# Optimization experiments

Measured on AMD Instinct MI355X. Metric: run time of the kernel, lower is better.

The kernel has to match this reference:

```python
import jax, jax.numpy as jnp
import numpy as np

B, T, D = 256, 512, 32   # batch, seq_len, var_length (== input_size == output_size)
H, L = 256, 2            # hidden_size, num_layers


def setup_inputs() -> dict:
    key = jax.random.key(0)
    ks = jax.random.split(key, 16)
    s = 1.0 / np.sqrt(H)  # PyTorch LSTM/Linear default init range
    def u(k, shape):
        return jax.random.uniform(k, shape, jnp.float32, -s, s)
    inp = {"input": jax.random.normal(ks[0], (B, T, D), jnp.float32)}
    # encoder LSTM (b = b_ih + b_hh folded together); gate order i,f,g,o
    inp["enc_Wih0"] = u(ks[1], (4 * H, D)); inp["enc_Whh0"] = u(ks[2], (4 * H, H)); inp["enc_b0"] = u(ks[3], (4 * H,))
    inp["enc_Wih1"] = u(ks[4], (4 * H, H)); inp["enc_Whh1"] = u(ks[5], (4 * H, H)); inp["enc_b1"] = u(ks[6], (4 * H,))
    # decoder LSTM
    inp["dec_Wih0"] = u(ks[7], (4 * H, D)); inp["dec_Whh0"] = u(ks[8], (4 * H, H)); inp["dec_b0"] = u(ks[9], (4 * H,))
    inp["dec_Wih1"] = u(ks[10], (4 * H, H)); inp["dec_Whh1"] = u(ks[11], (4 * H, H)); inp["dec_b1"] = u(ks[12], (4 * H,))
    # output projection
    inp["fc_W"] = u(ks[13], (D, H)); inp["fc_b"] = u(ks[14], (D,))
    return inp


def _lstm_cell(x, h, c, Wih, Whh, b):
    g = x @ Wih.T + h @ Whh.T + b            # [B, 4H]
    i, f, gg, o = jnp.split(g, 4, axis=-1)   # PyTorch gate order i,f,g,o
    c = jax.nn.sigmoid(f) * c + jax.nn.sigmoid(i) * jnp.tanh(gg)
    h = jax.nn.sigmoid(o) * jnp.tanh(c)
    return h, c


def reference(input, enc_Wih0, enc_Whh0, enc_b0, enc_Wih1, enc_Whh1, enc_b1,
              dec_Wih0, dec_Whh0, dec_b0, dec_Wih1, dec_Whh1, dec_b1, fc_W, fc_b):
    b, t, d = input.shape
    hdim = enc_Whh0.shape[1]
    x = jnp.transpose(input, (1, 0, 2))  # time-major [T, B, D]

    # ----- encoder: 2-layer LSTM, keep final (h, c) per layer -----
    enc = [(enc_Wih0, enc_Whh0, enc_b0), (enc_Wih1, enc_Whh1, enc_b1)]
    hs, cs = [], []
    seq = x
    for Wih, Whh, bb in enc:
        def step(carry, xt, Wih=Wih, Whh=Whh, bb=bb):
            h, c = carry
            h, c = _lstm_cell(xt, h, c, Wih, Whh, bb)
            return (h, c), h
        z = jnp.zeros((b, hdim), input.dtype)
        (hT, cT), seq = jax.lax.scan(step, (z, z), seq)
        hs.append(hT); cs.append(cT)
    h0 = jnp.stack(hs)  # [L, B, H]
    c0 = jnp.stack(cs)

    dec = [(dec_Wih0, dec_Whh0, dec_b0), (dec_Wih1, dec_Whh1, dec_b1)]

    def dec_step(carry, _):
        xt, h, c = carry
        inp_l = xt
        new_h, new_c = [], []
        for l, (Wih, Whh, bb) in enumerate(dec):
            hl, cl = _lstm_cell(inp_l, h[l], c[l], Wih, Whh, bb)
            new_h.append(hl); new_c.append(cl)
            inp_l = hl
        pred = inp_l @ fc_W.T + fc_b  # [B, D]
        return (pred, jnp.stack(new_h), jnp.stack(new_c)), pred

    x0 = jnp.zeros((b, d), input.dtype)
    _, preds = jax.lax.scan(dec_step, (x0, h0, c0), None, length=t)  # [T, B, D]
    # cat along time then reverse (inv_idx)
    out = jnp.transpose(preds, (1, 0, 2))[:, ::-1, :]
    return out
```

## Files before the change

### kernel.cpp

```cpp
#include <hip/hip_runtime.h>

typedef __attribute__((ext_vector_type(8))) short bf16x8;
typedef __attribute__((ext_vector_type(4))) float f32x4;

#define MFMA16(a,b,c) __builtin_amdgcn_mfma_f32_16x16x32_bf16((a),(b),(c),0,0,0)


#define SZ_HBUF   (2*256*256*2)
#define OFF_H0H   0
#define OFF_H0L   (OFF_H0H + SZ_HBUF)
#define OFF_H1H   (OFF_H0L + SZ_HBUF)
#define OFF_H1L   (OFF_H1H + SZ_HBUF)
#define OFF_CFIN  (OFF_H1L + SZ_HBUF)
#define OFF_EW0H  (OFF_CFIN + 524288)
#define OFF_EW0L  (OFF_EW0H + 589824)
#define OFF_EW1H  (OFF_EW0L + 589824)
#define OFF_EW1L  (OFF_EW1H + 1048576)
#define OFF_DW0H  (OFF_EW1L + 1048576)
#define OFF_DW0L  (OFF_DW0H + 1048576)
#define OFF_DW1H  (OFF_DW0L + 1048576)
#define OFF_DW1L  (OFF_DW1H + 1048576)
#define OFF_BEFF  (OFF_DW1L + 1048576)
#define OFF_FCWH  (OFF_BEFF + 4096)
#define OFF_FCWL  (OFF_FCWH + 16384)
#define OFF_EFLG  (OFF_FCWL + 16384)
#define OFF_DFLG  (OFF_EFLG + 4096)

static __device__ __forceinline__ unsigned short f2bf(float f) {
  unsigned u = __float_as_uint(f);
  u = u + 0x7fffu + ((u >> 16) & 1u);
  return (unsigned short)(u >> 16);
}
static __device__ __forceinline__ float bf2f(unsigned short s) {
  return __uint_as_float(((unsigned)s) << 16);
}
static __device__ __forceinline__ float sigf(float x) {
  return 1.f / (1.f + __expf(-x));
}
static __device__ __forceinline__ float tanhsafe(float x) {
  float a = fabsf(x);
  float e = __expf(-2.f * a);
  float t = (1.f - e) / (1.f + e);
  return x < 0.f ? -t : t;
}
static __device__ __forceinline__ void st_hpair(float h, unsigned short* ph, unsigned short* pl) {
  unsigned short hi = f2bf(h);
  unsigned short lo = f2bf(h - bf2f(hi));
  __hip_atomic_store(ph, hi, __ATOMIC_RELAXED, __HIP_MEMORY_SCOPE_AGENT);
  __hip_atomic_store(pl, lo, __ATOMIC_RELAXED, __HIP_MEMORY_SCOPE_AGENT);
}
static __device__ __forceinline__ f32x4 ld16(const void* p) {
  f32x4 d;
  asm volatile("global_load_dwordx4 %0, %1, off sc0 sc1" : "=&v"(d) : "v"(p) : "memory");
  return d;
}
static __device__ __forceinline__ void wait_vm0() {
  asm volatile("s_waitcnt vmcnt(0)" ::: "memory");
  __builtin_amdgcn_sched_barrier(0);
}
static __device__ __forceinline__ void flag_barrier(unsigned* flags, int gc, unsigned round) {
  __syncthreads();
  if (threadIdx.x == 0)
    __hip_atomic_store(flags + gc, round, __ATOMIC_RELAXED, __HIP_MEMORY_SCOPE_AGENT);
  if (threadIdx.x < 64) {
    int l = threadIdx.x;
    for (;;) {
      unsigned v = (l < 16) ? __hip_atomic_load(flags + l, __ATOMIC_RELAXED, __HIP_MEMORY_SCOPE_AGENT)
                            : round;
      if (__all((int)(v >= round))) break;
    }
  }
  __syncthreads();
}

#define LDSF(base, row, kk) \
  (*(const bf16x8*)((base) + ((((row) << 9) | (lrow << 4) | ((kk) << 6)) ^ (((row) & 7) << 4))))

__global__ void k_prep_cat(int nrows, const float* __restrict__ s0, int K0,
                           const float* __restrict__ s1, int K1,
                           unsigned short* __restrict__ whi, unsigned short* __restrict__ wlo) {
  int K = K0 + K1;
  int tot = nrows * K;
  for (int idx = blockIdx.x * blockDim.x + threadIdx.x; idx < tot; idx += gridDim.x * blockDim.x) {
    int n = idx / K, k = idx - n * K;
    float v = (k < K0) ? s0[n * K0 + k] : s1[n * K1 + (k - K0)];
    unsigned short hi = f2bf(v);
    unsigned short lo = f2bf(v - bf2f(hi));
    whi[idx] = hi; wlo[idx] = lo;
  }
}
__global__ void k_prep_dec0(const float* __restrict__ Wih0, const float* __restrict__ Whh0,
                            const float* __restrict__ fcW,
                            unsigned short* __restrict__ whi, unsigned short* __restrict__ wlo) {
  int tot = 1024 * 512;
  for (int idx = blockIdx.x * blockDim.x + threadIdx.x; idx < tot; idx += gridDim.x * blockDim.x) {
    int n = idx >> 9, k = idx & 511;
    float v;
    if (k < 256) {
      v = 0.f;
      #pragma unroll
      for (int d = 0; d < 32; ++d) v += Wih0[n * 32 + d] * fcW[d * 256 + k];
    } else {
      v = Whh0[n * 256 + (k - 256)];
    }
    unsigned short hi = f2bf(v);
    unsigned short lo = f2bf(v - bf2f(hi));
    whi[idx] = hi; wlo[idx] = lo;
  }
}
__global__ void k_prep_beff(const float* __restrict__ Wih0, const float* __restrict__ b0,
                            const float* __restrict__ fcb, float* __restrict__ beff) {
  int n = blockIdx.x * blockDim.x + threadIdx.x;
  if (n < 1024) {
    float v = b0[n];
    #pragma unroll
    for (int d = 0; d < 32; ++d) v += Wih0[n * 32 + d] * fcb[d];
    beff[n] = v;
  }
}

__global__ __launch_bounds__(256, 1)
void k_encoder(const float* __restrict__ input,
               const unsigned short* __restrict__ w0hi, const unsigned short* __restrict__ w0lo,
               const unsigned short* __restrict__ w1hi, const unsigned short* __restrict__ w1lo,
               const float* __restrict__ b0, const float* __restrict__ b1,
               unsigned short* h0h, unsigned short* h0l,
               unsigned short* h1h, unsigned short* h1l,
               float* __restrict__ cfin, unsigned* flags)
{
  const int wg = blockIdx.x;
  const int gb = wg & 15, gc = wg >> 4;
  const int tid = threadIdx.x;
  const int wid = tid >> 6, lane = tid & 63;
  const int lcol = lane & 15, lrow = lane >> 4;
  const int r0 = gb * 16, u0 = gc * 16;
  const int wrow = wid * 256 + u0 + lcol;

  __shared__ char s_h0[2][8192];
  __shared__ char s_h1[2][8192];
  __shared__ float gA[4][16][17];
  __shared__ float gB[4][16][17];
  __shared__ float cb[2][16][16];

  cb[0][tid >> 4][tid & 15] = 0.f;
  cb[1][tid >> 4][tid & 15] = 0.f;

  const int srow = (tid >> 5) & 7;
  const int scol8 = (tid & 31) << 3;
  const int dA = ((srow << 9) | ((tid & 31) << 4)) ^ (srow << 4);
  const int dB = dA + 4096;

  bf16x8 w0h_[9], w0l_[9], w1h_[16], w1l_[16];
  {
    const unsigned short* p = w0hi + (size_t)wrow * 288 + lrow * 8;
    const unsigned short* q = w0lo + (size_t)wrow * 288 + lrow * 8;
    #pragma unroll
    for (int kk = 0; kk < 9; ++kk) {
      w0h_[kk] = *(const bf16x8*)(p + kk * 32);
      w0l_[kk] = *(const bf16x8*)(q + kk * 32);
    }
    const unsigned short* p1 = w1hi + (size_t)wrow * 512 + lrow * 8;
    const unsigned short* q1 = w1lo + (size_t)wrow * 512 + lrow * 8;
    #pragma unroll
    for (int kk = 0; kk < 16; ++kk) {
      w1h_[kk] = *(const bf16x8*)(p1 + kk * 32);
      w1l_[kk] = *(const bf16x8*)(q1 + kk * 32);
    }
  }
  const float bias0 = b0[wrow];
  const float bias1 = b1[wrow];
  unsigned* gflags = flags + gb * 64;
  __syncthreads();

  for (int k = 0; k <= 512; ++k) {
    const int rp = (k - 1) & 1;
    const int wp = k & 1;

    f32x4 ahh = {0.f,0.f,0.f,0.f}, ahl = {0.f,0.f,0.f,0.f}, alh = {0.f,0.f,0.f,0.f};
    union { bf16x8 v; unsigned short s[8]; } xh, xl;
    if (k < 512) {
      const float* px = input + (size_t)(r0 + lcol) * 16384 + (size_t)k * 32 + lrow * 8;
      f32x4 a = *(const f32x4*)px;
      f32x4 b = *(const f32x4*)(px + 4);
      #pragma unroll
      for (int j = 0; j < 4; ++j) {
        unsigned short t1 = f2bf(a[j]); xh.s[j] = t1;     xl.s[j]     = f2bf(a[j] - bf2f(t1));
        unsigned short t2 = f2bf(b[j]); xh.s[4 + j] = t2; xl.s[4 + j] = f2bf(b[j] - bf2f(t2));
      }
    }

    const unsigned short* p0h = h0h + (size_t)rp * 65536 + (size_t)(r0 + srow) * 256 + scol8;
    const unsigned short* p0l = h0l + (size_t)rp * 65536 + (size_t)(r0 + srow) * 256 + scol8;
    const unsigned short* p1h = h1h + (size_t)wp * 65536 + (size_t)(r0 + srow) * 256 + scol8;
    const unsigned short* p1l = h1l + (size_t)wp * 65536 + (size_t)(r0 + srow) * 256 + scol8;
    f32x4 v0 = ld16(p0h), v1 = ld16(p0h + 2048);
    f32x4 v2 = ld16(p0l), v3 = ld16(p0l + 2048);
    f32x4 v4 = ld16(p1h), v5 = ld16(p1h + 2048);
    f32x4 v6 = ld16(p1l), v7 = ld16(p1l + 2048);

    if (k < 512) {
      ahh = MFMA16(xh.v, w0h_[0], ahh);
      ahl = MFMA16(xh.v, w0l_[0], ahl);
      alh = MFMA16(xl.v, w0h_[0], alh);
    }

    wait_vm0();
    *(f32x4*)(s_h0[0] + dA) = v0; *(f32x4*)(s_h0[0] + dB) = v1;
    *(f32x4*)(s_h0[1] + dA) = v2; *(f32x4*)(s_h0[1] + dB) = v3;
    *(f32x4*)(s_h1[0] + dA) = v4; *(f32x4*)(s_h1[0] + dB) = v5;
    *(f32x4*)(s_h1[1] + dA) = v6; *(f32x4*)(s_h1[1] + dB) = v7;
    __syncthreads();

    bf16x8 f0h[8], f0l[8];
    #pragma unroll
    for (int kk = 0; kk < 8; ++kk) {
      f0h[kk] = LDSF(s_h0[0], lcol, kk);
      f0l[kk] = LDSF(s_h0[1], lcol, kk);
    }

    if (k < 512) {
      #pragma unroll
      for (int kk = 0; kk < 8; ++kk) {
        ahh = MFMA16(f0h[kk], w0h_[kk + 1], ahh);
        ahl = MFMA16(f0h[kk], w0l_[kk + 1], ahl);
        alh = MFMA16(f0l[kk], w0h_[kk + 1], alh);
      }
      f32x4 g = ahh + ahl + alh;
      #pragma unroll
      for (int r = 0; r < 4; ++r) gA[wid][lrow * 4 + r][lcol] = g[r] + bias0;
    }
    if (k >= 1) {
      f32x4 bhh = {0.f,0.f,0.f,0.f}, bhl = {0.f,0.f,0.f,0.f}, blh = {0.f,0.f,0.f,0.f};
      #pragma unroll
      for (int kk = 0; kk < 8; ++kk) {
        bhh = MFMA16(f0h[kk], w1h_[kk], bhh);
        bhl = MFMA16(f0h[kk], w1l_[kk], bhl);
        blh = MFMA16(f0l[kk], w1h_[kk], blh);
      }
      #pragma unroll
      for (int kk = 0; kk < 8; ++kk) {
        bf16x8 fh_ = LDSF(s_h1[0], lcol, kk);
        bf16x8 fl_ = LDSF(s_h1[1], lcol, kk);
        bhh = MFMA16(fh_, w1h_[kk + 8], bhh);
        bhl = MFMA16(fh_, w1l_[kk + 8], bhl);
        blh = MFMA16(fl_, w1h_[kk + 8], blh);
      }
      f32x4 g = bhh + bhl + blh;
      #pragma unroll
      for (int r = 0; r < 4; ++r) gB[wid][lrow * 4 + r][lcol] = g[r] + bias1;
    }
    __syncthreads();

    const int urow = tid >> 4, uu = tid & 15;
    if (k < 512) {
      float gi = gA[0][urow][uu], gf = gA[1][urow][uu];
      float gg = gA[2][urow][uu], go = gA[3][urow][uu];
      float c = sigf(gf) * cb[0][urow][uu] + sigf(gi) * tanhsafe(gg);
      cb[0][urow][uu] = c;
      float h = sigf(go) * tanhsafe(c);
      size_t off = (size_t)wp * 65536 + (size_t)(r0 + urow) * 256 + (u0 + uu);
      st_hpair(h, h0h + off, h0l + off);
    }
    if (k >= 1) {
      float gi = gB[0][urow][uu], gf = gB[1][urow][uu];
      float gg = gB[2][urow][uu], go = gB[3][urow][uu];
      float c = sigf(gf) * cb[1][urow][uu] + sigf(gi) * tanhsafe(gg);
      cb[1][urow][uu] = c;
      float h = sigf(go) * tanhsafe(c);
      size_t off = (size_t)rp * 65536 + (size_t)(r0 + urow) * 256 + (u0 + uu);
      st_hpair(h, h1h + off, h1l + off);
    }
    flag_barrier(gflags, gc, (unsigned)(k + 1));
  }

  const int urow = tid >> 4, uu = tid & 15;
  cfin[(size_t)(r0 + urow) * 256 + (u0 + uu)] = cb[0][urow][uu];
  cfin[65536 + (size_t)(r0 + urow) * 256 + (u0 + uu)] = cb[1][urow][uu];
}

__global__ __launch_bounds__(256, 1)
void k_decoder(const unsigned short* __restrict__ w0hi, const unsigned short* __restrict__ w0lo,
               const unsigned short* __restrict__ w1hi, const unsigned short* __restrict__ w1lo,
               const float* __restrict__ beff, const float* __restrict__ db0,
               const float* __restrict__ b1, const float* __restrict__ fcb,
               const unsigned short* __restrict__ fcwh_g, const unsigned short* __restrict__ fcwl_g,
               unsigned short* h0h, unsigned short* h0l,
               unsigned short* h1h, unsigned short* h1l,
               const float* __restrict__ cfin, float* __restrict__ out, unsigned* flags)
{
  const int wg = blockIdx.x;
  const int gb = wg & 15, gc = wg >> 4;
  const int tid = threadIdx.x;
  const int wid = tid >> 6, lane = tid & 63;
  const int lcol = lane & 15, lrow = lane >> 4;
  const int r0 = gb * 16, u0 = gc * 16;
  const int wrow = wid * 256 + u0 + lcol;

  __shared__ char s_h1[2][8192];
  __shared__ char s_h0[2][2][8192];
  __shared__ char s_fcw[2][16384];
  __shared__ float gA[4][16][17];
  __shared__ float cb[2][16][16];

  const int srow = (tid >> 5) & 7;
  const int scol8 = (tid & 31) << 3;
  const int dA = ((srow << 9) | ((tid & 31) << 4)) ^ (srow << 4);
  const int dB = dA + 4096;

  {
    const int urow = tid >> 4, uu = tid & 15;
    cb[0][urow][uu] = cfin[(size_t)(r0 + urow) * 256 + (u0 + uu)];
    cb[1][urow][uu] = cfin[65536 + (size_t)(r0 + urow) * 256 + (u0 + uu)];
  }
  {
    const unsigned short* q1h = h1h + 65536 + (size_t)(r0 + srow) * 256 + scol8;
    const unsigned short* q1l = h1l + 65536 + (size_t)(r0 + srow) * 256 + scol8;
    const unsigned short* q0h = h0h + 65536 + (size_t)(r0 + srow) * 256 + scol8;
    const unsigned short* q0l = h0l + 65536 + (size_t)(r0 + srow) * 256 + scol8;
    f32x4 v0 = ld16(q1h), v1 = ld16(q1h + 2048);
    f32x4 v2 = ld16(q1l), v3 = ld16(q1l + 2048);
    f32x4 v4 = ld16(q0h), v5 = ld16(q0h + 2048);
    f32x4 v6 = ld16(q0l), v7 = ld16(q0l + 2048);
    f32x4 fh0 = ld16(fcwh_g + (size_t)srow * 256 + scol8);
    f32x4 fh1 = ld16(fcwh_g + (size_t)(srow + 8) * 256 + scol8);
    f32x4 fh2 = ld16(fcwh_g + (size_t)(srow + 16) * 256 + scol8);
    f32x4 fh3 = ld16(fcwh_g + (size_t)(srow + 24) * 256 + scol8);
    f32x4 fl0 = ld16(fcwl_g + (size_t)srow * 256 + scol8);
    f32x4 fl1 = ld16(fcwl_g + (size_t)(srow + 8) * 256 + scol8);
    f32x4 fl2 = ld16(fcwl_g + (size_t)(srow + 16) * 256 + scol8);
    f32x4 fl3 = ld16(fcwl_g + (size_t)(srow + 24) * 256 + scol8);
    wait_vm0();
    *(f32x4*)(s_h1[0] + dA) = v0;    *(f32x4*)(s_h1[0] + dB) = v1;
    *(f32x4*)(s_h1[1] + dA) = v2;    *(f32x4*)(s_h1[1] + dB) = v3;
    *(f32x4*)(s_h0[1][0] + dA) = v4; *(f32x4*)(s_h0[1][0] + dB) = v5;
    *(f32x4*)(s_h0[1][1] + dA) = v6; *(f32x4*)(s_h0[1][1] + dB) = v7;
    *(f32x4*)(s_fcw[0] + dA) = fh0;          *(f32x4*)(s_fcw[0] + dA + 4096) = fh1;
    *(f32x4*)(s_fcw[0] + dA + 8192) = fh2;   *(f32x4*)(s_fcw[0] + dA + 12288) = fh3;
    *(f32x4*)(s_fcw[1] + dA) = fl0;          *(f32x4*)(s_fcw[1] + dA + 4096) = fl1;
    *(f32x4*)(s_fcw[1] + dA + 8192) = fl2;   *(f32x4*)(s_fcw[1] + dA + 12288) = fl3;
  }

  bf16x8 w0h_[16], w0l_[16], w1h_[16], w1l_[16];
  {
    const unsigned short* p = w0hi + (size_t)wrow * 512 + lrow * 8;
    const unsigned short* q = w0lo + (size_t)wrow * 512 + lrow * 8;
    #pragma unroll
    for (int kk = 0; kk < 16; ++kk) {
      w0h_[kk] = *(const bf16x8*)(p + kk * 32);
      w0l_[kk] = *(const bf16x8*)(q + kk * 32);
    }
    const unsigned short* p1 = w1hi + (size_t)wrow * 512 + lrow * 8;
    const unsigned short* q1 = w1lo + (size_t)wrow * 512 + lrow * 8;
    #pragma unroll
    for (int kk = 0; kk < 16; ++kk) {
      w1h_[kk] = *(const bf16x8*)(p1 + kk * 32);
      w1l_[kk] = *(const bf16x8*)(q1 + kk * 32);
    }
  }
  const float bias0 = beff[wrow], bias0t0 = db0[wrow], bias1 = b1[wrow];
  const float fcbv = (wid < 2) ? fcb[wid * 16 + lcol] : 0.f;
  unsigned* gflags = flags + gb * 64;
  __syncthreads();

  bf16x8 h1h_r[8], h1l_r[8];

  for (int t = 0; t < 512; ++t) {
    const int wp = t & 1, rp = 1 - wp;

    f32x4 a0, a1, a2, a3;
    if (t > 0) {
      const unsigned short* ph = h1h + (size_t)rp * 65536 + (size_t)(r0 + srow) * 256 + scol8;
      const unsigned short* pl = h1l + (size_t)rp * 65536 + (size_t)(r0 + srow) * 256 + scol8;
      a0 = ld16(ph); a1 = ld16(ph + 2048);
      a2 = ld16(pl); a3 = ld16(pl + 2048);
    }
    f32x4 ahh = {0.f,0.f,0.f,0.f}, ahl = {0.f,0.f,0.f,0.f}, alh = {0.f,0.f,0.f,0.f};
    #pragma unroll
    for (int kk = 0; kk < 8; ++kk) {
      bf16x8 fh_ = LDSF(s_h0[rp][0], lcol, kk);
      bf16x8 fl_ = LDSF(s_h0[rp][1], lcol, kk);
      ahh = MFMA16(fh_, w0h_[kk + 8], ahh);
      ahl = MFMA16(fh_, w0l_[kk + 8], ahl);
      alh = MFMA16(fl_, w0h_[kk + 8], alh);
    }
    if (t > 0) {
      wait_vm0();
      *(f32x4*)(s_h1[0] + dA) = a0; *(f32x4*)(s_h1[0] + dB) = a1;
      *(f32x4*)(s_h1[1] + dA) = a2; *(f32x4*)(s_h1[1] + dB) = a3;
    }
    __syncthreads();
    #pragma unroll
    for (int kk = 0; kk < 8; ++kk) {
      h1h_r[kk] = LDSF(s_h1[0], lcol, kk);
      h1l_r[kk] = LDSF(s_h1[1], lcol, kk);
    }
    if (t > 0) {
      #pragma unroll
      for (int kk = 0; kk < 8; ++kk) {
        ahh = MFMA16(h1h_r[kk], w0h_[kk], ahh);
        ahl = MFMA16(h1h_r[kk], w0l_[kk], ahl);
        alh = MFMA16(h1l_r[kk], w0h_[kk], alh);
      }
    }
    {
      f32x4 g = ahh + ahl + alh;
      float bb = (t == 0) ? bias0t0 : bias0;
      #pragma unroll
      for (int r = 0; r < 4; ++r) gA[wid][lrow * 4 + r][lcol] = g[r] + bb;
    }
    __syncthreads();
    {
      const int urow = tid >> 4, uu = tid & 15;
      float gi = gA[0][urow][uu], gf = gA[1][urow][uu];
      float gg = gA[2][urow][uu], go = gA[3][urow][uu];
      float c = sigf(gf) * cb[0][urow][uu] + sigf(gi) * tanhsafe(gg);
      cb[0][urow][uu] = c;
      float h = sigf(go) * tanhsafe(c);
      size_t off = (size_t)wp * 65536 + (size_t)(r0 + urow) * 256 + (u0 + uu);
      st_hpair(h, h0h + off, h0l + off);
    }
    flag_barrier(gflags, gc, (unsigned)(2 * t + 1));

    f32x4 b0v, b1v, b2v, b3v;
    {
      const unsigned short* ph = h0h + (size_t)wp * 65536 + (size_t)(r0 + srow) * 256 + scol8;
      const unsigned short* pl = h0l + (size_t)wp * 65536 + (size_t)(r0 + srow) * 256 + scol8;
      b0v = ld16(ph); b1v = ld16(ph + 2048);
      b2v = ld16(pl); b3v = ld16(pl + 2048);
    }
    f32x4 bhh = {0.f,0.f,0.f,0.f}, bhl = {0.f,0.f,0.f,0.f}, blh = {0.f,0.f,0.f,0.f};
    #pragma unroll
    for (int kk = 0; kk < 8; ++kk) {
      bhh = MFMA16(h1h_r[kk], w1h_[kk + 8], bhh);
      bhl = MFMA16(h1h_r[kk], w1l_[kk + 8], bhl);
      blh = MFMA16(h1l_r[kk], w1h_[kk + 8], blh);
    }
    f32x4 p0 = {0.f,0.f,0.f,0.f}, p1 = {0.f,0.f,0.f,0.f}, p2 = {0.f,0.f,0.f,0.f};
    if (t > 0 && wid < 2) {
      #pragma unroll
      for (int kk = 0; kk < 8; ++kk) {
        bf16x8 fh_ = LDSF(s_fcw[0], wid * 16 + lcol, kk);
        bf16x8 fl_ = LDSF(s_fcw[1], wid * 16 + lcol, kk);
        p0 = MFMA16(h1h_r[kk], fh_, p0);
        p1 = MFMA16(h1h_r[kk], fl_, p1);
        p2 = MFMA16(h1l_r[kk], fh_, p2);
      }
    }
    wait_vm0();
    if (t > 0 && wid < 2 && gc == 0) {
      #pragma unroll
      for (int j = 0; j < 4; ++j)
        out[(size_t)(r0 + lrow * 4 + j) * 16384 + (size_t)(512 - t) * 32 + wid * 16 + lcol] =
            p0[j] + p1[j] + p2[j] + fcbv;
    }
    *(f32x4*)(s_h0[wp][0] + dA) = b0v; *(f32x4*)(s_h0[wp][0] + dB) = b1v;
    *(f32x4*)(s_h0[wp][1] + dA) = b2v; *(f32x4*)(s_h0[wp][1] + dB) = b3v;
    __syncthreads();
    {
      #pragma unroll
      for (int kk = 0; kk < 8; ++kk) {
        bf16x8 fh_ = LDSF(s_h0[wp][0], lcol, kk);
        bf16x8 fl_ = LDSF(s_h0[wp][1], lcol, kk);
        bhh = MFMA16(fh_, w1h_[kk], bhh);
        bhl = MFMA16(fh_, w1l_[kk], bhl);
        blh = MFMA16(fl_, w1h_[kk], blh);
      }
      f32x4 g = bhh + bhl + blh;
      #pragma unroll
      for (int r = 0; r < 4; ++r) gA[wid][lrow * 4 + r][lcol] = g[r] + bias1;
    }
    __syncthreads();
    {
      const int urow = tid >> 4, uu = tid & 15;
      float gi = gA[0][urow][uu], gf = gA[1][urow][uu];
      float gg = gA[2][urow][uu], go = gA[3][urow][uu];
      float c = sigf(gf) * cb[1][urow][uu] + sigf(gi) * tanhsafe(gg);
      cb[1][urow][uu] = c;
      float h = sigf(go) * tanhsafe(c);
      size_t off = (size_t)wp * 65536 + (size_t)(r0 + urow) * 256 + (u0 + uu);
      st_hpair(h, h1h + off, h1l + off);
    }
    flag_barrier(gflags, gc, (unsigned)(2 * t + 2));
  }

  {
    const unsigned short* ph = h1h + 65536 + (size_t)(r0 + srow) * 256 + scol8;
    const unsigned short* pl = h1l + 65536 + (size_t)(r0 + srow) * 256 + scol8;
    f32x4 v0 = ld16(ph), v1 = ld16(ph + 2048);
    f32x4 v2 = ld16(pl), v3 = ld16(pl + 2048);
    wait_vm0();
    *(f32x4*)(s_h1[0] + dA) = v0; *(f32x4*)(s_h1[0] + dB) = v1;
    *(f32x4*)(s_h1[1] + dA) = v2; *(f32x4*)(s_h1[1] + dB) = v3;
  }
  __syncthreads();
  if (wid < 2) {
    f32x4 p0 = {0.f,0.f,0.f,0.f}, p1 = {0.f,0.f,0.f,0.f}, p2 = {0.f,0.f,0.f,0.f};
    #pragma unroll
    for (int kk = 0; kk < 8; ++kk) {
      bf16x8 ah = LDSF(s_h1[0], lcol, kk);
      bf16x8 al = LDSF(s_h1[1], lcol, kk);
      bf16x8 fh_ = LDSF(s_fcw[0], wid * 16 + lcol, kk);
      bf16x8 fl_ = LDSF(s_fcw[1], wid * 16 + lcol, kk);
      p0 = MFMA16(ah, fh_, p0);
      p1 = MFMA16(ah, fl_, p1);
      p2 = MFMA16(al, fh_, p2);
    }
    if (gc == 0) {
      #pragma unroll
      for (int j = 0; j < 4; ++j)
        out[(size_t)(r0 + lrow * 4 + j) * 16384 + wid * 16 + lcol] = p0[j] + p1[j] + p2[j] + fcbv;
    }
  }
}

extern "C" void kernel_launch(void* const* d_in, const int* in_sizes, int n_in,
                              void* d_out, int out_size, void* d_ws, size_t ws_size,
                              hipStream_t stream) {
  (void)in_sizes; (void)n_in; (void)ws_size;
  const float* input = (const float*)d_in[0];
  const float* eWih0 = (const float*)d_in[1];
  const float* eWhh0 = (const float*)d_in[2];
  const float* eb0   = (const float*)d_in[3];
  const float* eWih1 = (const float*)d_in[4];
  const float* eWhh1 = (const float*)d_in[5];
  const float* eb1   = (const float*)d_in[6];
  const float* dWih0 = (const float*)d_in[7];
  const float* dWhh0 = (const float*)d_in[8];
  const float* db0   = (const float*)d_in[9];
  const float* dWih1 = (const float*)d_in[10];
  const float* dWhh1 = (const float*)d_in[11];
  const float* db1   = (const float*)d_in[12];
  const float* fcW   = (const float*)d_in[13];
  const float* fcb   = (const float*)d_in[14];

  char* ws = (char*)d_ws;
  unsigned short* h0h = (unsigned short*)(ws + OFF_H0H);
  unsigned short* h0l = (unsigned short*)(ws + OFF_H0L);
  unsigned short* h1h = (unsigned short*)(ws + OFF_H1H);
  unsigned short* h1l = (unsigned short*)(ws + OFF_H1L);
  float* cfin = (float*)(ws + OFF_CFIN);
  unsigned short* ew0h = (unsigned short*)(ws + OFF_EW0H);
  unsigned short* ew0l = (unsigned short*)(ws + OFF_EW0L);
  unsigned short* ew1h = (unsigned short*)(ws + OFF_EW1H);
  unsigned short* ew1l = (unsigned short*)(ws + OFF_EW1L);
  unsigned short* dw0h = (unsigned short*)(ws + OFF_DW0H);
  unsigned short* dw0l = (unsigned short*)(ws + OFF_DW0L);
  unsigned short* dw1h = (unsigned short*)(ws + OFF_DW1H);
  unsigned short* dw1l = (unsigned short*)(ws + OFF_DW1L);
  float* beff = (float*)(ws + OFF_BEFF);
  unsigned short* fcwh = (unsigned short*)(ws + OFF_FCWH);
  unsigned short* fcwl = (unsigned short*)(ws + OFF_FCWL);
  unsigned* eflg = (unsigned*)(ws + OFF_EFLG);
  unsigned* dflg = (unsigned*)(ws + OFF_DFLG);

  hipMemsetAsync(d_out, 0, (size_t)out_size * sizeof(float), stream);
  hipMemsetAsync(ws + OFF_H0H, 0, (size_t)4 * SZ_HBUF, stream);
  hipMemsetAsync(ws + OFF_EFLG, 0, 8192, stream);

  k_prep_cat<<<1024, 256, 0, stream>>>(1024, eWih0, 32,  eWhh0, 256, ew0h, ew0l);
  k_prep_cat<<<1024, 256, 0, stream>>>(1024, eWih1, 256, eWhh1, 256, ew1h, ew1l);
  k_prep_cat<<<1024, 256, 0, stream>>>(1024, dWih1, 256, dWhh1, 256, dw1h, dw1l);
  k_prep_cat<<<64, 256, 0, stream>>>(32, fcW, 256, fcW, 0, fcwh, fcwl);
  k_prep_dec0<<<1024, 256, 0, stream>>>(dWih0, dWhh0, fcW, dw0h, dw0l);
  k_prep_beff<<<4, 256, 0, stream>>>(dWih0, db0, fcb, beff);

  k_encoder<<<256, 256, 0, stream>>>(input, ew0h, ew0l, ew1h, ew1l, eb0, eb1,
                                     h0h, h0l, h1h, h1l, cfin, eflg);
  k_decoder<<<256, 256, 0, stream>>>(dw0h, dw0l, dw1h, dw1l, beff, db0, db1, fcb,
                                     fcwh, fcwl, h0h, h0l, h1h, h1l, cfin,
                                     (float*)d_out, dflg);
}
```

Baseline: 4.125 ms.

## Keep LSTM gate math in registers via lane shuffles, removing LDS gate staging

```diff
diff --git a/kernel.cpp b/kernel.cpp
--- a/kernel.cpp
+++ b/kernel.cpp
@@ -73,6 +73,27 @@
   __syncthreads();
 }
 
+static __device__ __forceinline__ void xpose4(float g0, float g1, float g2, float g3, int q,
+                                              float& o0, float& o1, float& o2, float& o3) {
+  const bool b0 = (q & 1) != 0, b1 = (q & 2) != 0;
+  float s01 = b0 ? g0 : g1;
+  float s23 = b0 ? g2 : g3;
+  float r01 = __shfl_xor(s01, 1);
+  float r23 = __shfl_xor(s23, 1);
+  float C0 = b0 ? r01 : g0;
+  float C1 = b0 ? g1 : r01;
+  float C2 = b0 ? r23 : g2;
+  float C3 = b0 ? g3 : r23;
+  float s02 = b1 ? C0 : C2;
+  float s13 = b1 ? C1 : C3;
+  float r02 = __shfl_xor(s02, 2);
+  float r13 = __shfl_xor(s13, 2);
+  o0 = b1 ? r02 : C0;
+  o1 = b1 ? r13 : C1;
+  o2 = b1 ? C2 : r02;
+  o3 = b1 ? C3 : r13;
+}
+
 #define LDSF(base, row, kk) \
   (*(const bf16x8*)((base) + ((((row) << 9) | (lrow << 4) | ((kk) << 6)) ^ (((row) & 7) << 4))))
 
@@ -134,16 +155,14 @@
   const int wid = tid >> 6, lane = tid & 63;
   const int lcol = lane & 15, lrow = lane >> 4;
   const int r0 = gb * 16, u0 = gc * 16;
-  const int wrow = wid * 256 + u0 + lcol;
+  const int q = lcol & 3, ul = lcol >> 2;
+  const int wrow = q * 256 + u0 + wid * 4 + ul;
+  const int myb = r0 + lrow * 4 + q;
+  const int myu = u0 + wid * 4 + ul;
+  const size_t myoff = (size_t)myb * 256 + myu;
 
   __shared__ char s_h0[2][8192];
   __shared__ char s_h1[2][8192];
-  __shared__ float gA[4][16][17];
-  __shared__ float gB[4][16][17];
-  __shared__ float cb[2][16][16];
-
-  cb[0][tid >> 4][tid & 15] = 0.f;
-  cb[1][tid >> 4][tid & 15] = 0.f;
 
   const int srow = (tid >> 5) & 7;
   const int scol8 = (tid & 31) << 3;
@@ -153,11 +172,11 @@
   bf16x8 w0h_[9], w0l_[9], w1h_[16], w1l_[16];
   {
     const unsigned short* p = w0hi + (size_t)wrow * 288 + lrow * 8;
-    const unsigned short* q = w0lo + (size_t)wrow * 288 + lrow * 8;
+    const unsigned short* qq = w0lo + (size_t)wrow * 288 + lrow * 8;
     #pragma unroll
     for (int kk = 0; kk < 9; ++kk) {
       w0h_[kk] = *(const bf16x8*)(p + kk * 32);
-      w0l_[kk] = *(const bf16x8*)(q + kk * 32);
+      w0l_[kk] = *(const bf16x8*)(qq + kk * 32);
     }
     const unsigned short* p1 = w1hi + (size_t)wrow * 512 + lrow * 8;
     const unsigned short* q1 = w1lo + (size_t)wrow * 512 + lrow * 8;
@@ -169,25 +188,25 @@
   }
   const float bias0 = b0[wrow];
   const float bias1 = b1[wrow];
+  float c0reg = 0.f, c1reg = 0.f;
   unsigned* gflags = flags + gb * 64;
+
+  const float* pxrow = input + (size_t)(r0 + lcol) * 16384 + lrow * 8;
+  union { bf16x8 v; unsigned short s[8]; } xh, xl;
+  {
+    f32x4 a = *(const f32x4*)(pxrow);
+    f32x4 b = *(const f32x4*)(pxrow + 4);
+    #pragma unroll
+    for (int j = 0; j < 4; ++j) {
+      unsigned short t1 = f2bf(a[j]); xh.s[j] = t1;     xl.s[j]     = f2bf(a[j] - bf2f(t1));
+      unsigned short t2 = f2bf(b[j]); xh.s[4 + j] = t2; xl.s[4 + j] = f2bf(b[j] - bf2f(t2));
+    }
+  }
   __syncthreads();
 
   for (int k = 0; k <= 512; ++k) {
     const int rp = (k - 1) & 1;
     const int wp = k & 1;
-
-    f32x4 ahh = {0.f,0.f,0.f,0.f}, ahl = {0.f,0.f,0.f,0.f}, alh = {0.f,0.f,0.f,0.f};
-    union { bf16x8 v; unsigned short s[8]; } xh, xl;
-    if (k < 512) {
-      const float* px = input + (size_t)(r0 + lcol) * 16384 + (size_t)k * 32 + lrow * 8;
-      f32x4 a = *(const f32x4*)px;
-      f32x4 b = *(const f32x4*)(px + 4);
-      #pragma unroll
-      for (int j = 0; j < 4; ++j) {
-        unsigned short t1 = f2bf(a[j]); xh.s[j] = t1;     xl.s[j]     = f2bf(a[j] - bf2f(t1));
-        unsigned short t2 = f2bf(b[j]); xh.s[4 + j] = t2; xl.s[4 + j] = f2bf(b[j] - bf2f(t2));
-      }
-    }
 
     const unsigned short* p0h = h0h + (size_t)rp * 65536 + (size_t)(r0 + srow) * 256 + scol8;
     const unsigned short* p0l = h0l + (size_t)rp * 65536 + (size_t)(r0 + srow) * 256 + scol8;
@@ -197,7 +216,13 @@
     f32x4 v2 = ld16(p0l), v3 = ld16(p0l + 2048);
     f32x4 v4 = ld16(p1h), v5 = ld16(p1h + 2048);
     f32x4 v6 = ld16(p1l), v7 = ld16(p1l + 2048);
-
+    f32x4 nxa, nxb;
+    if (k < 511) {
+      nxa = ld16(pxrow + (size_t)(k + 1) * 32);
+      nxb = ld16(pxrow + (size_t)(k + 1) * 32 + 4);
+    }
+
+    f32x4 ahh = {0.f,0.f,0.f,0.f}, ahl = {0.f,0.f,0.f,0.f}, alh = {0.f,0.f,0.f,0.f};
     if (k < 512) {
       ahh = MFMA16(xh.v, w0h_[0], ahh);
       ahl = MFMA16(xh.v, w0l_[0], ahl);
@@ -209,6 +234,13 @@
     *(f32x4*)(s_h0[1] + dA) = v2; *(f32x4*)(s_h0[1] + dB) = v3;
     *(f32x4*)(s_h1[0] + dA) = v4; *(f32x4*)(s_h1[0] + dB) = v5;
     *(f32x4*)(s_h1[1] + dA) = v6; *(f32x4*)(s_h1[1] + dB) = v7;
+    if (k < 511) {
+      #pragma unroll
+      for (int j = 0; j < 4; ++j) {
+        unsigned short t1 = f2bf(nxa[j]); xh.s[j] = t1;     xl.s[j]     = f2bf(nxa[j] - bf2f(t1));
+        unsigned short t2 = f2bf(nxb[j]); xh.s[4 + j] = t2; xl.s[4 + j] = f2bf(nxb[j] - bf2f(t2));
+      }
+    }
     __syncthreads();
 
     bf16x8 f0h[8], f0l[8];
@@ -226,8 +258,13 @@
         alh = MFMA16(f0l[kk], w0h_[kk + 1], alh);
       }
       f32x4 g = ahh + ahl + alh;
-      #pragma unroll
-      for (int r = 0; r < 4; ++r) gA[wid][lrow * 4 + r][lcol] = g[r] + bias0;
+      float gi, gf, gg, go;
+      xpose4(g[0] + bias0, g[1] + bias0, g[2] + bias0, g[3] + bias0, q, gi, gf, gg, go);
+      float c = sigf(gf) * c0reg + sigf(gi) * tanhsafe(gg);
+      c0reg = c;
+      float h = sigf(go) * tanhsafe(c);
+      size_t off = (size_t)wp * 65536 + myoff;
+      st_hpair(h, h0h + off, h0l + off);
     }
     if (k >= 1) {
       f32x4 bhh = {0.f,0.f,0.f,0.f}, bhl = {0.f,0.f,0.f,0.f}, blh = {0.f,0.f,0.f,0.f};
@@ -246,36 +283,19 @@
         blh = MFMA16(fl_, w1h_[kk + 8], blh);
       }
       f32x4 g = bhh + bhl + blh;
-      #pragma unroll
-      for (int r = 0; r < 4; ++r) gB[wid][lrow * 4 + r][lcol] = g[r] + bias1;
-    }
-    __syncthreads();
-
-    const int urow = tid >> 4, uu = tid & 15;
-    if (k < 512) {
-      float gi = gA[0][urow][uu], gf = gA[1][urow][uu];
-      float gg = gA[2][urow][uu], go = gA[3][urow][uu];
-      float c = sigf(gf) * cb[0][urow][uu] + sigf(gi) * tanhsafe(gg);
-      cb[0][urow][uu] = c;
+      float gi, gf, gg, go;
+      xpose4(g[0] + bias1, g[1] + bias1, g[2] + bias1, g[3] + bias1, q, gi, gf, gg, go);
+      float c = sigf(gf) * c1reg + sigf(gi) * tanhsafe(gg);
+      c1reg = c;
       float h = sigf(go) * tanhsafe(c);
-      size_t off = (size_t)wp * 65536 + (size_t)(r0 + urow) * 256 + (u0 + uu);
-      st_hpair(h, h0h + off, h0l + off);
-    }
-    if (k >= 1) {
-      float gi = gB[0][urow][uu], gf = gB[1][urow][uu];
-      float gg = gB[2][urow][uu], go = gB[3][urow][uu];
-      float c = sigf(gf) * cb[1][urow][uu] + sigf(gi) * tanhsafe(gg);
-      cb[1][urow][uu] = c;
-      float h = sigf(go) * tanhsafe(c);
-      size_t off = (size_t)rp * 65536 + (size_t)(r0 + urow) * 256 + (u0 + uu);
+      size_t off = (size_t)rp * 65536 + myoff;
       st_hpair(h, h1h + off, h1l + off);
     }
     flag_barrier(gflags, gc, (unsigned)(k + 1));
   }
 
-  const int urow = tid >> 4, uu = tid & 15;
-  cfin[(size_t)(r0 + urow) * 256 + (u0 + uu)] = cb[0][urow][uu];
-  cfin[65536 + (size_t)(r0 + urow) * 256 + (u0 + uu)] = cb[1][urow][uu];
+  cfin[myoff] = c0reg;
+  cfin[65536 + myoff] = c1reg;
 }
 
 __global__ __launch_bounds__(256, 1)
@@ -294,29 +314,28 @@
   const int wid = tid >> 6, lane = tid & 63;
   const int lcol = lane & 15, lrow = lane >> 4;
   const int r0 = gb * 16, u0 = gc * 16;
-  const int wrow = wid * 256 + u0 + lcol;
+  const int q = lcol & 3, ul = lcol >> 2;
+  const int wrow = q * 256 + u0 + wid * 4 + ul;
+  const size_t myoff = (size_t)(r0 + lrow * 4 + q) * 256 + (u0 + wid * 4 + ul);
 
   __shared__ char s_h1[2][8192];
   __shared__ char s_h0[2][2][8192];
   __shared__ char s_fcw[2][16384];
-  __shared__ float gA[4][16][17];
-  __shared__ float cb[2][16][16];
 
   const int srow = (tid >> 5) & 7;
   const int scol8 = (tid & 31) << 3;
   const int dA = ((srow << 9) | ((tid & 31) << 4)) ^ (srow << 4);
   const int dB = dA + 4096;
 
+  float c0reg = cfin[myoff];
+  float c1reg = cfin[65536 + myoff];
+
+  const size_t rowoff = (size_t)(r0 + srow) * 256 + scol8;
   {
-    const int urow = tid >> 4, uu = tid & 15;
-    cb[0][urow][uu] = cfin[(size_t)(r0 + urow) * 256 + (u0 + uu)];
-    cb[1][urow][uu] = cfin[65536 + (size_t)(r0 + urow) * 256 + (u0 + uu)];
-  }
-  {
-    const unsigned short* q1h = h1h + 65536 + (size_t)(r0 + srow) * 256 + scol8;
-    const unsigned short* q1l = h1l + 65536 + (size_t)(r0 + srow) * 256 + scol8;
-    const unsigned short* q0h = h0h + 65536 + (size_t)(r0 + srow) * 256 + scol8;
-    const unsigned short* q0l = h0l + 65536 + (size_t)(r0 + srow) * 256 + scol8;
+    const unsigned short* q1h = h1h + 65536 + rowoff;
+    const unsigned short* q1l = h1l + 65536 + rowoff;
+    const unsigned short* q0h = h0h + 65536 + rowoff;
+    const unsigned short* q0l = h0l + 65536 + rowoff;
     f32x4 v0 = ld16(q1h), v1 = ld16(q1h + 2048);
     f32x4 v2 = ld16(q1l), v3 = ld16(q1l + 2048);
     f32x4 v4 = ld16(q0h), v5 = ld16(q0h + 2048);
@@ -343,11 +362,11 @@
   bf16x8 w0h_[16], w0l_[16], w1h_[16], w1l_[16];
   {
     const unsigned short* p = w0hi + (size_t)wrow * 512 + lrow * 8;
-    const unsigned short* q = w0lo + (size_t)wrow * 512 + lrow * 8;
+    const unsigned short* qq = w0lo + (size_t)wrow * 512 + lrow * 8;
     #pragma unroll
     for (int kk = 0; kk < 16; ++kk) {
       w0h_[kk] = *(const bf16x8*)(p + kk * 32);
-      w0l_[kk] = *(const bf16x8*)(q + kk * 32);
+      w0l_[kk] = *(const bf16x8*)(qq + kk * 32);
     }
     const unsigned short* p1 = w1hi + (size_t)wrow * 512 + lrow * 8;
     const unsigned short* q1 = w1lo + (size_t)wrow * 512 + lrow * 8;
@@ -360,6 +379,10 @@
   const float bias0 = beff[wrow], bias0t0 = db0[wrow], bias1 = b1[wrow];
   const float fcbv = (wid < 2) ? fcb[wid * 16 + lcol] : 0.f;
   unsigned* gflags = flags + gb * 64;
+  const unsigned short* h1h_p0 = h1h + rowoff; const unsigned short* h1h_p1 = h1h + 65536 + rowoff;
+  const unsigned short* h1l_p0 = h1l + rowoff; const unsigned short* h1l_p1 = h1l + 65536 + rowoff;
+  const unsigned short* h0h_p0 = h0h + rowoff; const unsigned short* h0h_p1 = h0h + 65536 + rowoff;
+  const unsigned short* h0l_p0 = h0l + rowoff; const unsigned short* h0l_p1 = h0l + 65536 + rowoff;
   __syncthreads();
 
   bf16x8 h1h_r[8], h1l_r[8];
@@ -369,8 +392,8 @@
 
     f32x4 a0, a1, a2, a3;
     if (t > 0) {
-      const unsigned short* ph = h1h + (size_t)rp * 65536 + (size_t)(r0 + srow) * 256 + scol8;
-      const unsigned short* pl = h1l + (size_t)rp * 65536 + (size_t)(r0 + srow) * 256 + scol8;
+      const unsigned short* ph = rp ? h1h_p1 : h1h_p0;
+      const unsigned short* pl = rp ? h1l_p1 : h1l_p0;
       a0 = ld16(ph); a1 = ld16(ph + 2048);
       a2 = ld16(pl); a3 = ld16(pl + 2048);
     }
@@ -405,26 +428,20 @@
     {
       f32x4 g = ahh + ahl + alh;
       float bb = (t == 0) ? bias0t0 : bias0;
-      #pragma unroll
-      for (int r = 0; r < 4; ++r) gA[wid][lrow * 4 + r][lcol] = g[r] + bb;
-    }
-    __syncthreads();
-    {
-      const int urow = tid >> 4, uu = tid & 15;
-      float gi = gA[0][urow][uu], gf = gA[1][urow][uu];
-      float gg = gA[2][urow][uu], go = gA[3][urow][uu];
-      float c = sigf(gf) * cb[0][urow][uu] + sigf(gi) * tanhsafe(gg);
-      cb[0][urow][uu] = c;
+      float gi, gf, gg, go;
+      xpose4(g[0] + bb, g[1] + bb, g[2] + bb, g[3] + bb, q, gi, gf, gg, go);
+      float c = sigf(gf) * c0reg + sigf(gi) * tanhsafe(gg);
+      c0reg = c;
       float h = sigf(go) * tanhsafe(c);
-      size_t off = (size_t)wp * 65536 + (size_t)(r0 + urow) * 256 + (u0 + uu);
+      size_t off = (size_t)wp * 65536 + myoff;
       st_hpair(h, h0h + off, h0l + off);
     }
     flag_barrier(gflags, gc, (unsigned)(2 * t + 1));
 
     f32x4 b0v, b1v, b2v, b3v;
     {
-      const unsigned short* ph = h0h + (size_t)wp * 65536 + (size_t)(r0 + srow) * 256 + scol8;
-      const unsigned short* pl = h0l + (size_t)wp * 65536 + (size_t)(r0 + srow) * 256 + scol8;
+      const unsigned short* ph = wp ? h0h_p1 : h0h_p0;
+      const unsigned short* pl = wp ? h0l_p1 : h0l_p0;
       b0v = ld16(ph); b1v = ld16(ph + 2048);
       b2v = ld16(pl); b3v = ld16(pl + 2048);
     }
@@ -466,28 +483,20 @@
         blh = MFMA16(fl_, w1h_[kk], blh);
       }
       f32x4 g = bhh + bhl + blh;
-      #pragma unroll
-      for (int r = 0; r < 4; ++r) gA[wid][lrow * 4 + r][lcol] = g[r] + bias1;
-    }
-    __syncthreads();
-    {
-      const int urow = tid >> 4, uu = tid & 15;
-      float gi = gA[0][urow][uu], gf = gA[1][urow][uu];
-      float gg = gA[2][urow][uu], go = gA[3][urow][uu];
-      float c = sigf(gf) * cb[1][urow][uu] + sigf(gi) * tanhsafe(gg);
-      cb[1][urow][uu] = c;
+      float gi, gf, gg, go;
+      xpose4(g[0] + bias1, g[1] + bias1, g[2] + bias1, g[3] + bias1, q, gi, gf, gg, go);
+      float c = sigf(gf) * c1reg + sigf(gi) * tanhsafe(gg);
+      c1reg = c;
       float h = sigf(go) * tanhsafe(c);
-      size_t off = (size_t)wp * 65536 + (size_t)(r0 + urow) * 256 + (u0 + uu);
+      size_t off = (size_t)wp * 65536 + myoff;
       st_hpair(h, h1h + off, h1l + off);
     }
     flag_barrier(gflags, gc, (unsigned)(2 * t + 2));
   }
 
   {
-    const unsigned short* ph = h1h + 65536 + (size_t)(r0 + srow) * 256 + scol8;
-    const unsigned short* pl = h1l + 65536 + (size_t)(r0 + srow) * 256 + scol8;
-    f32x4 v0 = ld16(ph), v1 = ld16(ph + 2048);
-    f32x4 v2 = ld16(pl), v3 = ld16(pl + 2048);
+    f32x4 v0 = ld16(h1h_p1), v1 = ld16(h1h_p1 + 2048);
+    f32x4 v2 = ld16(h1l_p1), v3 = ld16(h1l_p1 + 2048);
     wait_vm0();
     *(f32x4*)(s_h1[0] + dA) = v0; *(f32x4*)(s_h1[0] + dB) = v1;
     *(f32x4*)(s_h1[1] + dA) = v2; *(f32x4*)(s_h1[1] + dB) = v3;
```

Measured after the change: 4.299 ms. 4.2% more time.
